# Kernel tuning notes

Hardware: AMD Instinct MI355X
Metric: run time of the kernel (lower is better)

Reference implementation:

```python
import jax, jax.numpy as jnp
import numpy as np

EPS = 1e-8

def _normalize(x, eps=EPS):
    mean = jnp.mean(x, axis=-1, keepdims=True)
    var = jnp.var(x, axis=-1, keepdims=True)  # unbiased=False
    return (x - mean) / jnp.sqrt(var + eps)


def setup_inputs() -> dict:
    key = jax.random.key(0)
    ks = jax.random.split(key, 10)
    B, M, d = 8, 50000, 256
    out_units, num_heads, gsl_hidden = 256, 8, 16
    s = 0.02
    return {
        "h": jax.random.normal(ks[0], (B, M, d), dtype=jnp.float32),
        "att_w": jax.random.normal(ks[1], (d, num_heads), dtype=jnp.float32) * s,
        "att_b": jnp.zeros((num_heads,), dtype=jnp.float32),
        "w_w": jax.random.normal(ks[2], (d, out_units), dtype=jnp.float32) * s,
        "res_w": jax.random.normal(ks[3], (d, out_units), dtype=jnp.float32) * s,
        "res_b": jnp.zeros((out_units,), dtype=jnp.float32),
        "gsl1_w": jax.random.normal(ks[4], (d, gsl_hidden), dtype=jnp.float32) * s,
        "gsl1_b": jnp.zeros((gsl_hidden,), dtype=jnp.float32),
        "gsl2_w": jax.random.normal(ks[5], (gsl_hidden, 1), dtype=jnp.float32) * s,
        "gsl2_b": jnp.zeros((1,), dtype=jnp.float32),
        "k": 500,
    }


def reference(h, att_w, att_b, w_w, res_w, res_b, gsl1_w, gsl1_b, gsl2_w, gsl2_b, k):
    B, M, d = h.shape
    num_heads = att_w.shape[1]
    out_units = w_w.shape[1]
    head_dim = out_units // num_heads

    # additive attention scores per head: [B, M, H]
    A = jax.nn.relu(jnp.einsum('bmd,dh->bmh', h, att_w) + att_b)
    # value projection: [B, M, out]
    H_lin = jnp.einsum('bmd,de->bme', h, w_w)

    # learned graph-structure-learning scores: [B, M]
    S_hidden = jax.nn.relu(jnp.einsum('bmd,dg->bmg', h, gsl1_w) + gsl1_b)
    S = jax.nn.sigmoid(jnp.einsum('bmg,go->bmo', S_hidden, gsl2_w) + gsl2_b)[..., 0]

    # top-k mask over nodes (dim=1)
    k_eff = min(k, M)
    topk_vals, _ = jax.lax.top_k(S, k_eff)  # sorted descending
    kth = topk_vals[:, -1:]                 # [B, 1]
    mask = (S >= kth).astype(h.dtype)       # [B, M]

    # masked scores (zeros at masked positions, NOT -inf: faithful to source)
    A_mod = A * mask[:, :, None]            # [B, M, H]
    weights = jax.nn.softmax(A_mod, axis=1)  # softmax over M per head
    # (dropout is a no-op in eval mode)

    # per-head weighted sum over nodes, then concat heads along feature dim
    Hr = H_lin.reshape(B, M, num_heads, head_dim)
    out = jnp.einsum('bmh,bmhd->bhd', weights, Hr).reshape(B, 1, out_units)

    # residual from mean-pooled input
    Q_res = jax.nn.relu(jnp.einsum('bmd,de->bme', jnp.mean(h, axis=1, keepdims=True), res_w) + res_b)
    out = jax.nn.relu(out + Q_res)
    return _normalize(out), mask[:, None, :]
```

## Files before the change

### kernel.cpp

```cpp
#include <hip/hip_runtime.h>
#include <cstdint>
#include <cstddef>


#define MM     50000
#define BATCH  8
#define TILES  196
#define CH     8
#define NCHUNK 32
#define CANDCAP 4096
#define COMPCAP 2048

#define OFF_Z      0u
#define OFF_CANDR  1600000u
#define OFF_CANDK  1731072u
#define OFF_COMP   1993216u
#define OFF_LO     2058752u
#define OFF_PAD    2058784u
#define OFF_SUMH   2058848u
#define OFF_UCORR  2075232u
#define OFF_ZCORR  2206304u
#define OFF_CCNT   2206816u
#define OFF_CANDC  2206848u
#define ZERO_OFF   OFF_SUMH
#define ZERO_SZ    148032u

__device__ __forceinline__ unsigned int f32_sortable(float z) {
    unsigned int u = __float_as_uint(z);
    return (u & 0x80000000u) ? ~u : (u | 0x80000000u);
}

__global__ __launch_bounds__(256) void k1_main(
    const float* __restrict__ h,
    const float* __restrict__ g1w,
    const float* __restrict__ g1b,
    const float* __restrict__ g2w,
    const float* __restrict__ g2b,
    float* __restrict__ z32,
    double* __restrict__ sumh)
{
    __shared__ float tile[4][CH][65];
    __shared__ float lsum[256];

    const int tid  = threadIdx.x;
    const int w    = tid >> 6;
    const int lane = tid & 63;
    lsum[tid] = 0.0f;
    __syncthreads();

    const int bid = blockIdx.x;
    const int b   = bid / TILES;
    const int t0  = bid % TILES;
    const int wave_row0 = t0 * 256 + w * 64;
    const size_t bbase = (size_t)b * MM;

    const int kq   = lane & 1;
    const int rsub = lane >> 1;

    float gacc[16];
#pragma unroll
    for (int g = 0; g < 16; ++g) gacc[g] = 0.0f;

    const int m0 = wave_row0 + rsub;
    const int m1 = wave_row0 + 32 + rsub;
    const size_t r0c = bbase + (size_t)((m0 < MM) ? m0 : (MM - 1));
    const size_t r1c = bbase + (size_t)((m1 < MM) ? m1 : (MM - 1));

    {
        float4 v0 = *(const float4*)(h + r0c * 256 + kq * 4);
        float4 v1 = *(const float4*)(h + r1c * 256 + kq * 4);
        if (m0 >= MM) { v0.x = v0.y = v0.z = v0.w = 0.f; }
        if (m1 >= MM) { v1.x = v1.y = v1.z = v1.w = 0.f; }
        tile[w][kq*4+0][rsub] = v0.x;  tile[w][kq*4+1][rsub] = v0.y;
        tile[w][kq*4+2][rsub] = v0.z;  tile[w][kq*4+3][rsub] = v0.w;
        tile[w][kq*4+0][32+rsub] = v1.x;  tile[w][kq*4+1][32+rsub] = v1.y;
        tile[w][kq*4+2][32+rsub] = v1.z;  tile[w][kq*4+3][32+rsub] = v1.w;
    }

    for (int c = 0; c < NCHUNK; ++c) {
        float4 n0, n1;
        const bool has = (c + 1 < NCHUNK);
        if (has) {
            const int kof = (c + 1) * CH + kq * 4;
            n0 = *(const float4*)(h + r0c * 256 + kof);
            n1 = *(const float4*)(h + r1c * 256 + kof);
            if (m0 >= MM) { n0.x = n0.y = n0.z = n0.w = 0.f; }
            if (m1 >= MM) { n1.x = n1.y = n1.z = n1.w = 0.f; }
        }
        const int k0 = c * CH;
#pragma unroll
        for (int kk = 0; kk < CH; ++kk) {
            float hv = tile[w][kk][lane];
            const float* gw = g1w + (k0 + kk) * 16;
#pragma unroll
            for (int g = 0; g < 16; ++g) gacc[g] = fmaf(hv, gw[g], gacc[g]);
        }
        {
            const int dsub = lane & 7;
            const int rq   = lane >> 3;
            float s = 0.f;
#pragma unroll
            for (int i = 0; i < 8; ++i) s += tile[w][dsub][rq * 8 + i];
            s += __shfl_xor(s, 8, 64);
            s += __shfl_xor(s, 16, 64);
            s += __shfl_xor(s, 32, 64);
            if (lane < 8) atomicAdd(&lsum[k0 + lane], s);
        }
        if (has) {
            tile[w][kq*4+0][rsub] = n0.x;  tile[w][kq*4+1][rsub] = n0.y;
            tile[w][kq*4+2][rsub] = n0.z;  tile[w][kq*4+3][rsub] = n0.w;
            tile[w][kq*4+0][32+rsub] = n1.x;  tile[w][kq*4+1][32+rsub] = n1.y;
            tile[w][kq*4+2][32+rsub] = n1.z;  tile[w][kq*4+3][32+rsub] = n1.w;
        }
    }

    const int m = wave_row0 + lane;
    if (m < MM) {
        float z = g2b[0];
#pragma unroll
        for (int g = 0; g < 16; ++g) {
            float sg = gacc[g] + g1b[g];
            sg = fmaxf(sg, 0.0f);
            z = fmaf(sg, g2w[g], z);
        }
        z32[bbase + m] = z;
    }
    __syncthreads();
    atomicAdd(&sumh[b * 256 + tid], (double)lsum[tid]);
}

__global__ __launch_bounds__(1024) void k2_sample(
    const float* __restrict__ z32,
    const int* __restrict__ kptr,
    unsigned int* __restrict__ lo_out)
{
    __shared__ unsigned int buf[1024];
    const int b   = blockIdx.x;
    const int tid = threadIdx.x;
    const size_t base = (size_t)b * MM;
    const int kval = min(*kptr, MM);

    int idx = (int)(((long long)tid * MM) / 1024);
    buf[tid] = f32_sortable(z32[base + idx]);
    __syncthreads();
    for (int sz = 2; sz <= 1024; sz <<= 1)
        for (int j = sz >> 1; j > 0; j >>= 1) {
            __syncthreads();
            int i = tid, ixj = i ^ j;
            if (ixj > i) {
                unsigned int a = buf[i], c = buf[ixj];
                bool up = ((i & sz) == 0);
                if ((up && a > c) || (!up && a < c)) { buf[i] = c; buf[ixj] = a; }
            }
        }
    __syncthreads();
    if (tid == 0) {
        int ks = (int)(((long long)kval * 1024) / MM) + 35;
        ks = min(1023, max(1, ks));
        lo_out[b] = buf[1023 - ks];
    }
}

__global__ __launch_bounds__(256) void k3_band(
    const float* __restrict__ z32,
    const unsigned int* __restrict__ lo_in,
    float* __restrict__ maskout,
    int* __restrict__ cand_cnt,
    int* __restrict__ cand_rows)
{
    int bid = blockIdx.x;
    int b = bid / TILES, t0 = bid % TILES;
    int m = t0 * 256 + threadIdx.x;
    int lane = threadIdx.x & 63;
    bool cand = false;
    if (m < MM) {
        size_t row = (size_t)b * MM + m;
        cand = (f32_sortable(z32[row]) >= lo_in[b]);
        if (!cand) maskout[row] = 0.0f;
    }
    unsigned long long ball = __ballot(cand);
    int wbase = 0;
    if (lane == 0) { int wc = __popcll(ball); if (wc) wbase = atomicAdd(&cand_cnt[b], wc); }
    wbase = __shfl(wbase, 0, 64);
    if (cand) {
        int pos = wbase + __popcll(ball & ((1ull << lane) - 1ull));
        if (pos < CANDCAP) cand_rows[b * CANDCAP + pos] = m;
    }
}

__global__ __launch_bounds__(256) void k3r_refine(
    const float* __restrict__ h,
    const float* __restrict__ g1w,
    const float* __restrict__ g1b,
    const float* __restrict__ g2w,
    const float* __restrict__ g2b,
    const int* __restrict__ cand_cnt,
    const int* __restrict__ cand_rows,
    unsigned long long* __restrict__ cand_keys)
{
    __shared__ double g1s[256][16];
    const int b    = blockIdx.x >> 4;
    const int part = blockIdx.x & 15;
    const int tid  = threadIdx.x;
    for (int i = tid; i < 4096; i += 256) g1s[i >> 4][i & 15] = (double)g1w[i];
    __syncthreads();

    const int n = min(cand_cnt[b], CANDCAP);
    const size_t bbase = (size_t)b * MM;
    for (int slot = part * 256 + tid; slot < n; slot += 4096) {
        int row = cand_rows[b * CANDCAP + slot];
        const float* hp = h + (bbase + (size_t)row) * 256;
        double gacc[16];
#pragma unroll
        for (int g = 0; g < 16; ++g) gacc[g] = 0.0;
        for (int k = 0; k < 256; ++k) {
            double hd = (double)hp[k];
#pragma unroll
            for (int g = 0; g < 16; ++g) gacc[g] = fma(hd, g1s[k][g], gacc[g]);
        }
        double z = (double)g2b[0];
#pragma unroll
        for (int g = 0; g < 16; ++g) {
            double sg = gacc[g] + (double)g1b[g];
            sg = sg > 0.0 ? sg : 0.0;
            z = fma(sg, (double)g2w[g], z);
        }
        long long uz = __double_as_longlong(z);
        unsigned long long key = (uz < 0)
            ? ~((unsigned long long)uz)
            : ((unsigned long long)uz | 0x8000000000000000ULL);
        cand_keys[b * CANDCAP + slot] = key;
    }
}

__global__ __launch_bounds__(1024) void k3s_select(
    const int* __restrict__ kptr,
    const int* __restrict__ cand_cnt,
    const int* __restrict__ cand_rows,
    const unsigned long long* __restrict__ cand_keys,
    float* __restrict__ maskout,
    int* __restrict__ ccnt,
    int* __restrict__ compact)
{
    __shared__ unsigned long long kbuf[CANDCAP];
    __shared__ int s_cnt;

    const int b    = blockIdx.x;
    const int tid  = threadIdx.x;
    const int lane = tid & 63;
    const int n = min(cand_cnt[b], CANDCAP);
    const size_t bbase = (size_t)b * MM;
    int kval = min(*kptr, MM);
    if (kval > n) kval = n;

    for (int i = tid; i < n; i += 1024) kbuf[i] = cand_keys[b * CANDCAP + i];
    __syncthreads();

    unsigned long long p64 = 0;
    int kk = kval;
    for (int bit = 63; bit >= 0; --bit) {
        if (tid == 0) s_cnt = 0;
        __syncthreads();
        unsigned long long himask = (bit == 63) ? 0ull : (~0ull << (bit + 1));
        int loc = 0;
        for (int i = tid; i < n; i += 1024) {
            unsigned long long x = kbuf[i];
            if (((x ^ p64) & himask) == 0ull && ((x >> bit) & 1ull)) loc++;
        }
        loc += __shfl_xor(loc, 32, 64);
        loc += __shfl_xor(loc, 16, 64);
        loc += __shfl_xor(loc, 8, 64);
        loc += __shfl_xor(loc, 4, 64);
        loc += __shfl_xor(loc, 2, 64);
        loc += __shfl_xor(loc, 1, 64);
        if (lane == 0 && loc) atomicAdd(&s_cnt, loc);
        __syncthreads();
        int c1 = s_cnt;
        if (c1 >= kk) p64 |= (1ull << bit); else kk -= c1;
        __syncthreads();
    }

    for (int i0 = 0; i0 < n; i0 += 1024) {
        int i = i0 + tid;
        bool active = (i < n);
        bool mk = false;
        int row = 0;
        if (active) {
            row = cand_rows[b * CANDCAP + i];
            mk = (kbuf[i] >= p64);
            maskout[bbase + row] = mk ? 1.0f : 0.0f;
        }
        unsigned long long ball = __ballot(mk);
        int wbase = 0;
        if (lane == 0) { int wc = __popcll(ball); if (wc) wbase = atomicAdd(&ccnt[b], wc); }
        wbase = __shfl(wbase, 0, 64);
        if (mk) {
            int pos = wbase + __popcll(ball & ((1ull << lane) - 1ull));
            if (pos < COMPCAP) compact[b * COMPCAP + pos] = row;
        }
    }
}

__global__ __launch_bounds__(256) void k4_corr(
    const float* __restrict__ h,
    const float* __restrict__ att_w,
    const float* __restrict__ att_b,
    const int* __restrict__ compact,
    const int* __restrict__ ccnt,
    double* __restrict__ Ucorr,
    double* __restrict__ Zcorr)
{
    __shared__ float hv_s[256];
    __shared__ float a_s[8];

    const int b    = blockIdx.x >> 5;
    const int part = blockIdx.x & 31;
    const int tid  = threadIdx.x;
    const int head = tid >> 5;
    const int seg  = tid & 31;
    const size_t bbase = (size_t)b * MM;
    const int n = min(ccnt[b], COMPCAP);

    float acc[8], zac[8];
#pragma unroll
    for (int j = 0; j < 8; ++j) { acc[j] = 0.f; zac[j] = 0.f; }

    for (int i = part; i < n; i += 32) {
        int row = compact[b * COMPCAP + i];
        float hv = h[(bbase + (size_t)row) * 256 + tid];
        hv_s[tid] = hv;
        __syncthreads();
        float p = 0.f;
#pragma unroll
        for (int j = 0; j < 8; ++j)
            p = fmaf(hv_s[seg * 8 + j], att_w[(seg * 8 + j) * 8 + head], p);
        p += __shfl_xor(p, 1, 64);
        p += __shfl_xor(p, 2, 64);
        p += __shfl_xor(p, 4, 64);
        p += __shfl_xor(p, 8, 64);
        p += __shfl_xor(p, 16, 64);
        if (seg == 0) a_s[head] = fmaxf(p + att_b[head], 0.f);
        __syncthreads();
#pragma unroll
        for (int j = 0; j < 8; ++j) {
            float w8 = expf(a_s[j]) - 1.0f;
            acc[j] = fmaf(w8, hv, acc[j]);
            zac[j] += w8;
        }
        __syncthreads();
    }
#pragma unroll
    for (int j = 0; j < 8; ++j)
        atomicAdd(&Ucorr[(b * 8 + j) * 256 + tid], (double)acc[j]);
    if (tid == 0) {
#pragma unroll
        for (int j = 0; j < 8; ++j) atomicAdd(&Zcorr[b * 8 + j], (double)zac[j]);
    }
}

__global__ __launch_bounds__(256) void k5_final(
    const double* __restrict__ sumh,
    const double* __restrict__ Ucorr,
    const double* __restrict__ Zcorr,
    const int* __restrict__ ccnt,
    const float* __restrict__ w_w,
    const float* __restrict__ res_w,
    const float* __restrict__ res_b,
    float* __restrict__ out0)
{
    __shared__ float Us[8 * 256];
    __shared__ float ms[256];
    __shared__ float red[256];
    __shared__ float s_mean, s_var;

    int b = blockIdx.x, e = threadIdx.x;
    double sh = sumh[b * 256 + e];
    ms[e] = (float)sh;
#pragma unroll
    for (int j = 0; j < 8; ++j)
        Us[j * 256 + e] = (float)(sh + Ucorr[(b * 8 + j) * 256 + e]);
    __syncthreads();

    int hh = e >> 5;
    float Z = (float)((double)(MM - ccnt[b]) + Zcorr[b * 8 + hh]);
    float attn = 0.f, qr = 0.f;
    for (int d = 0; d < 256; ++d) {
        attn = fmaf(Us[hh * 256 + d], w_w[d * 256 + e], attn);
        qr   = fmaf(ms[d],            res_w[d * 256 + e], qr);
    }
    float qres = fmaxf(qr * (1.0f / (float)MM) + res_b[e], 0.f);
    float pre  = fmaxf(attn / Z + qres, 0.f);

    red[e] = pre; __syncthreads();
    for (int s = 128; s > 0; s >>= 1) { if (e < s) red[e] += red[e + s]; __syncthreads(); }
    if (e == 0) s_mean = red[0] * (1.0f / 256.0f);
    __syncthreads();
    float mean = s_mean;
    float dv = pre - mean;
    red[e] = dv * dv; __syncthreads();
    for (int s = 128; s > 0; s >>= 1) { if (e < s) red[e] += red[e + s]; __syncthreads(); }
    if (e == 0) s_var = red[0] * (1.0f / 256.0f);
    __syncthreads();
    out0[b * 256 + e] = dv / sqrtf(s_var + 1e-8f);
}

extern "C" void kernel_launch(void* const* d_in, const int* in_sizes, int n_in,
                              void* d_out, int out_size, void* d_ws, size_t ws_size,
                              hipStream_t stream) {
    const float* h     = (const float*)d_in[0];
    const float* att_w = (const float*)d_in[1];
    const float* att_b = (const float*)d_in[2];
    const float* w_w   = (const float*)d_in[3];
    const float* res_w = (const float*)d_in[4];
    const float* res_b = (const float*)d_in[5];
    const float* g1w   = (const float*)d_in[6];
    const float* g1b   = (const float*)d_in[7];
    const float* g2w   = (const float*)d_in[8];
    const float* g2b   = (const float*)d_in[9];
    const int*   kptr  = (const int*)d_in[10];

    char* ws = (char*)d_ws;
    float*              z32     = (float*)(ws + OFF_Z);
    int*                candr   = (int*)(ws + OFF_CANDR);
    unsigned long long* candk   = (unsigned long long*)(ws + OFF_CANDK);
    int*                compact = (int*)(ws + OFF_COMP);
    unsigned int*       lo      = (unsigned int*)(ws + OFF_LO);
    double*             sumh    = (double*)(ws + OFF_SUMH);
    double*             Ucorr   = (double*)(ws + OFF_UCORR);
    double*             Zcorr   = (double*)(ws + OFF_ZCORR);
    int*                ccnt    = (int*)(ws + OFF_CCNT);
    int*                candc   = (int*)(ws + OFF_CANDC);

    float* out0    = (float*)d_out;
    float* maskout = out0 + BATCH * 256;

    hipMemsetAsync(ws + ZERO_OFF, 0, ZERO_SZ, stream);

    k1_main   <<<BATCH*TILES, 256,  0, stream>>>(h, g1w, g1b, g2w, g2b, z32, sumh);
    k2_sample <<<BATCH,       1024, 0, stream>>>(z32, kptr, lo);
    k3_band   <<<BATCH*TILES, 256,  0, stream>>>(z32, lo, maskout, candc, candr);
    k3r_refine<<<BATCH*16,    256,  0, stream>>>(h, g1w, g1b, g2w, g2b,
                                                 candc, candr, candk);
    k3s_select<<<BATCH,       1024, 0, stream>>>(kptr, candc, candr, candk,
                                                 maskout, ccnt, compact);
    k4_corr   <<<BATCH*32,    256,  0, stream>>>(h, att_w, att_b, compact, ccnt,
                                                 Ucorr, Zcorr);
    k5_final  <<<BATCH,       256,  0, stream>>>(sumh, Ucorr, Zcorr, ccnt,
                                                 w_w, res_w, res_b, out0);
}
```

Measured before the change: 828.6 us.

## Widen k1 chunk to 32 columns with 128-byte coalesced row loads

Restructures the k1 gating/column-sum kernel so each wave loads 32-column chunks (8 lanes × float4 per row, 8 rows per lane) instead of 8-column chunks. Each row read becomes a full 128-byte segment, there are fewer chunk iterations, and more loads are in flight per lane. Column sums are now computed from registers with shuffles rather than re-read from shared memory. In exchange it uses more registers for the load buffer, a 4x larger shared tile, and more atomics per chunk.

```diff
diff --git a/kernel.cpp b/kernel.cpp
--- a/kernel.cpp
+++ b/kernel.cpp
@@ -6,8 +6,6 @@
 #define MM     50000
 #define BATCH  8
 #define TILES  196
-#define CH     8
-#define NCHUNK 32
 #define CANDCAP 4096
 #define COMPCAP 2048
 
@@ -39,7 +37,7 @@
     float* __restrict__ z32,
     double* __restrict__ sumh)
 {
-    __shared__ float tile[4][CH][65];
+    __shared__ float tile[4][32][65];
     __shared__ float lsum[256];
 
     const int tid  = threadIdx.x;
@@ -54,65 +52,89 @@
     const int wave_row0 = t0 * 256 + w * 64;
     const size_t bbase = (size_t)b * MM;
 
-    const int kq   = lane & 1;
-    const int rsub = lane >> 1;
+    const int subrow = lane >> 3;
+    const int colq   = lane & 7;
+
+    const float* rp[8];
+    bool valid[8];
+#pragma unroll
+    for (int i = 0; i < 8; ++i) {
+        const int m = wave_row0 + subrow + 8 * i;
+        valid[i] = (m < MM);
+        const int mc = valid[i] ? m : (MM - 1);
+        rp[i] = h + (bbase + (size_t)mc) * 256 + colq * 4;
+    }
+
+    float4 buf[8];
+
+#define K1_LOAD(cc) do {                                                    \
+    _Pragma("unroll")                                                       \
+    for (int i = 0; i < 8; ++i) {                                           \
+        float4 v = *(const float4*)(rp[i] + (cc) * 32);                     \
+        if (!valid[i]) { v.x = 0.f; v.y = 0.f; v.z = 0.f; v.w = 0.f; }      \
+        buf[i] = v;                                                         \
+    }                                                                       \
+} while (0)
+
+#define K1_CSUM(cc) do {                                                    \
+    float sx = 0.f, sy = 0.f, sz = 0.f, sw = 0.f;                           \
+    _Pragma("unroll")                                                       \
+    for (int i = 0; i < 8; ++i) {                                           \
+        sx += buf[i].x; sy += buf[i].y; sz += buf[i].z; sw += buf[i].w;     \
+    }                                                                       \
+    sx += __shfl_xor(sx, 8, 64);  sy += __shfl_xor(sy, 8, 64);              \
+    sz += __shfl_xor(sz, 8, 64);  sw += __shfl_xor(sw, 8, 64);              \
+    sx += __shfl_xor(sx, 16, 64); sy += __shfl_xor(sy, 16, 64);             \
+    sz += __shfl_xor(sz, 16, 64); sw += __shfl_xor(sw, 16, 64);             \
+    sx += __shfl_xor(sx, 32, 64); sy += __shfl_xor(sy, 32, 64);             \
+    sz += __shfl_xor(sz, 32, 64); sw += __shfl_xor(sw, 32, 64);             \
+    if (subrow == 0) {                                                      \
+        atomicAdd(&lsum[(cc) * 32 + colq * 4 + 0], sx);                     \
+        atomicAdd(&lsum[(cc) * 32 + colq * 4 + 1], sy);                     \
+        atomicAdd(&lsum[(cc) * 32 + colq * 4 + 2], sz);                     \
+        atomicAdd(&lsum[(cc) * 32 + colq * 4 + 3], sw);                     \
+    }                                                                       \
+} while (0)
+
+#define K1_STORE() do {                                                     \
+    _Pragma("unroll")                                                       \
+    for (int i = 0; i < 8; ++i) {                                           \
+        const int rr = subrow + 8 * i;                                      \
+        tile[w][colq * 4 + 0][rr] = buf[i].x;                               \
+        tile[w][colq * 4 + 1][rr] = buf[i].y;                               \
+        tile[w][colq * 4 + 2][rr] = buf[i].z;                               \
+        tile[w][colq * 4 + 3][rr] = buf[i].w;                               \
+    }                                                                       \
+} while (0)
 
     float gacc[16];
 #pragma unroll
     for (int g = 0; g < 16; ++g) gacc[g] = 0.0f;
 
-    const int m0 = wave_row0 + rsub;
-    const int m1 = wave_row0 + 32 + rsub;
-    const size_t r0c = bbase + (size_t)((m0 < MM) ? m0 : (MM - 1));
-    const size_t r1c = bbase + (size_t)((m1 < MM) ? m1 : (MM - 1));
-
-    {
-        float4 v0 = *(const float4*)(h + r0c * 256 + kq * 4);
-        float4 v1 = *(const float4*)(h + r1c * 256 + kq * 4);
-        if (m0 >= MM) { v0.x = v0.y = v0.z = v0.w = 0.f; }
-        if (m1 >= MM) { v1.x = v1.y = v1.z = v1.w = 0.f; }
-        tile[w][kq*4+0][rsub] = v0.x;  tile[w][kq*4+1][rsub] = v0.y;
-        tile[w][kq*4+2][rsub] = v0.z;  tile[w][kq*4+3][rsub] = v0.w;
-        tile[w][kq*4+0][32+rsub] = v1.x;  tile[w][kq*4+1][32+rsub] = v1.y;
-        tile[w][kq*4+2][32+rsub] = v1.z;  tile[w][kq*4+3][32+rsub] = v1.w;
-    }
-
-    for (int c = 0; c < NCHUNK; ++c) {
-        float4 n0, n1;
-        const bool has = (c + 1 < NCHUNK);
+    K1_LOAD(0);
+    K1_CSUM(0);
+    K1_STORE();
+
+    for (int c = 0; c < 8; ++c) {
+        const bool has = (c < 7);
+        if (has) K1_LOAD(c + 1);
+        const int k0 = c * 32;
+#pragma unroll
+        for (int kk = 0; kk < 32; ++kk) {
+            const float hv = tile[w][kk][lane];
+            const float* gw = g1w + (k0 + kk) * 16;
+#pragma unroll
+            for (int g = 0; g < 16; ++g) gacc[g] = fmaf(hv, gw[g], gacc[g]);
+        }
         if (has) {
-            const int kof = (c + 1) * CH + kq * 4;
-            n0 = *(const float4*)(h + r0c * 256 + kof);
-            n1 = *(const float4*)(h + r1c * 256 + kof);
-            if (m0 >= MM) { n0.x = n0.y = n0.z = n0.w = 0.f; }
-            if (m1 >= MM) { n1.x = n1.y = n1.z = n1.w = 0.f; }
-        }
-        const int k0 = c * CH;
-#pragma unroll
-        for (int kk = 0; kk < CH; ++kk) {
-            float hv = tile[w][kk][lane];
-            const float* gw = g1w + (k0 + kk) * 16;
-#pragma unroll
-            for (int g = 0; g < 16; ++g) gacc[g] = fmaf(hv, gw[g], gacc[g]);
-        }
-        {
-            const int dsub = lane & 7;
-            const int rq   = lane >> 3;
-            float s = 0.f;
-#pragma unroll
-            for (int i = 0; i < 8; ++i) s += tile[w][dsub][rq * 8 + i];
-            s += __shfl_xor(s, 8, 64);
-            s += __shfl_xor(s, 16, 64);
-            s += __shfl_xor(s, 32, 64);
-            if (lane < 8) atomicAdd(&lsum[k0 + lane], s);
-        }
-        if (has) {
-            tile[w][kq*4+0][rsub] = n0.x;  tile[w][kq*4+1][rsub] = n0.y;
-            tile[w][kq*4+2][rsub] = n0.z;  tile[w][kq*4+3][rsub] = n0.w;
-            tile[w][kq*4+0][32+rsub] = n1.x;  tile[w][kq*4+1][32+rsub] = n1.y;
-            tile[w][kq*4+2][32+rsub] = n1.z;  tile[w][kq*4+3][32+rsub] = n1.w;
-        }
-    }
+            K1_CSUM(c + 1);
+            K1_STORE();
+        }
+    }
+
+#undef K1_LOAD
+#undef K1_CSUM
+#undef K1_STORE
 
     const int m = wave_row0 + lane;
     if (m < MM) {
```

Result: slower. 885.0 us (+6.8%).
